# Kernel tuning notes

Measured on AMD Instinct MI355X. Metric: run time of the kernel, lower is better.

## Reference

```python
import jax, jax.numpy as jnp
import numpy as np

PI = np.pi
NDIMS, K, M, F = 3, 513, 65536, 16
H = (K - 1) // 2  # 256; augmented factor has K = 2*H + 1 rows


def setup_inputs() -> dict:
    key = jax.random.key(0)
    k1, k2, k3, k4 = jax.random.split(key, 4)
    x = jax.random.uniform(k1, (M, NDIMS), dtype=jnp.float32)          # samples in [0,1]
    factors_real = jax.random.uniform(k2, (NDIMS, H, F), dtype=jnp.float32)
    factors_imag = 0.1 * jax.random.uniform(k3, (NDIMS, H, F), dtype=jnp.float32)
    lam = jnp.full((F,), 1.0 / F, dtype=jnp.float32)                   # f_vec init in torch
    return {"x": x, "factors_real": factors_real, "factors_imag": factors_imag, "lam": lam}


def _augment(fr, fi):
    # aug_fac real = [R; ones; flip(R)], imag = [I; zeros; -flip(I)]  -> (NDIMS, K, F)
    ones = jnp.ones((NDIMS, 1, F), fr.dtype)
    zeros = jnp.zeros((NDIMS, 1, F), fi.dtype)
    Ar = jnp.concatenate([fr, ones, jnp.flip(fr, axis=1)], axis=1)
    Ai = jnp.concatenate([fi, zeros, -jnp.flip(fi, axis=1)], axis=1)
    return Ar, Ai


def _conditionals(Ar, Ai):
    # c[n, f] = 1 / trapz(relu(Re(bb1^T aug_fac_n))[:, f], t),  t = linspace(0.01, 1, 100)
    T = 100
    t = jnp.linspace(0.01, 1.0, T, dtype=jnp.float32)
    kv = jnp.arange(-H, H + 1, dtype=jnp.float32)
    phi = (2.0 * PI) * kv[:, None] * t[None, :]                         # (K, T)
    # bb1 = exp(-i*phi): Re(bb1^T (Ar + i Ai)) = cos(phi)^T Ar + sin(phi)^T Ai
    y = (jnp.einsum('kt,nkf->ntf', jnp.cos(phi), Ar)
         + jnp.einsum('kt,nkf->ntf', jnp.sin(phi), Ai))
    y = jnp.maximum(y, 0.0)
    dt = jnp.float32((1.0 - 0.01) / (T - 1))
    integral = 0.5 * jnp.sum(y[:, 1:, :] + y[:, :-1, :], axis=1) * dt   # (NDIMS, F)
    return 1.0 / integral


def reference(x, factors_real, factors_imag, lam):
    Ar, Ai = _augment(factors_real, factors_imag)
    # torch computes c from detached data (numpy trapz) -> constant w.r.t. grads
    c = jax.lax.stop_gradient(_conditionals(Ar, Ai))                    # (NDIMS, F)
    kv = jnp.arange(-H, H + 1, dtype=jnp.float32)
    # basis = exp(-i*2pi*k*x): Re(basis^T A) = cos^T Ar + sin^T Ai
    theta = (2.0 * PI) * kv[None, :, None] * jnp.swapaxes(x, 0, 1)[:, None, :]  # (NDIMS, K, M)
    proj = (jnp.einsum('nkm,nkf->nmf', jnp.cos(theta), Ar)
            + jnp.einsum('nkm,nkf->nmf', jnp.sin(theta), Ai))           # (NDIMS, M, F)
    proj = jnp.maximum(proj, 0.0) * c[:, None, :]
    res = jnp.prod(proj, axis=0)                                        # (M, F)
    # sum(res @ diagflat(lam), dim=1) == res @ lam
    return res @ lam
```

## Files before the change

### kernel.cpp

```cpp
#include <hip/hip_runtime.h>

#define NDIMS 3
#define H_HALF 256
#define F_DIM 16
#define PI_F 3.14159265358979323846f

typedef _Float16 half8_t __attribute__((ext_vector_type(8)));
typedef _Float16 h2 __attribute__((ext_vector_type(2)));
typedef __fp16 pk2_t __attribute__((ext_vector_type(2)));
typedef float float4_t __attribute__((ext_vector_type(4)));

#if __has_builtin(__builtin_amdgcn_fractf)
#define FRACT1(u) __builtin_amdgcn_fractf(u)
#else
#define FRACT1(u) ((u) - floorf(u))
#endif
#if __has_builtin(__builtin_amdgcn_sinf)
#define SIN2PI(u) __builtin_amdgcn_sinf(u)
#define COS2PI(u) __builtin_amdgcn_cosf(u)
#else
#define SIN2PI(u) __sinf(6.283185307f * (u))
#define COS2PI(u) __cosf(6.283185307f * (u))
#endif

static __device__ __forceinline__ unsigned int pk(float lo, float hi) {
    const pk2_t p = __builtin_amdgcn_cvt_pkrtz(lo, hi);
    return __builtin_bit_cast(unsigned int, p);
}
static __device__ __forceinline__ h2 pkh(float lo, float hi) {
    const pk2_t p = __builtin_amdgcn_cvt_pkrtz(lo, hi);
    return __builtin_bit_cast(h2, p);
}

__global__ __launch_bounds__(256) void cond_partial_kernel(const float* __restrict__ fr,
                                                           const float* __restrict__ fi,
                                                           float* __restrict__ part_out) {
    const int n = blockIdx.x / 7;
    const int chunk = blockIdx.x % 7;
    const int tid = threadIdx.x;
    const int f = tid & 15;
    const int tq = tid >> 4;
    const int t_idx = chunk * 16 + tq;
    const float t = 0.01f + 0.01f * (float)t_idx;
    const float beta = 2.f * PI_F * t;
    const float cb = __cosf(beta), sb = __sinf(beta);
    float cj = cb, sj = sb;
    const float* frn = fr + n * H_HALF * F_DIM + f;
    const float* fin = fi + n * H_HALF * F_DIM + f;
    float acc = 0.f;
    #pragma unroll 8
    for (int j = 1; j <= H_HALF; ++j) {
        const int h = H_HALF - j;
        acc = fmaf(cj, frn[h * F_DIM], acc);
        acc = fmaf(-sj, fin[h * F_DIM], acc);
        const float cn = fmaf(cj, cb, -sj * sb);
        const float sn = fmaf(sj, cb, cj * sb);
        cj = cn; sj = sn;
    }
    const float y = fmaxf(fmaf(2.f, acc, 1.f), 0.f);
    const float wgt = (t_idx == 0 || t_idx == 99) ? 0.005f : 0.01f;
    float contrib = (t_idx < 100) ? wgt * y : 0.f;
    contrib += __shfl_xor(contrib, 16, 64);
    contrib += __shfl_xor(contrib, 32, 64);
    __shared__ float red[4][16];
    const int wv = tid >> 6;
    const int lane = tid & 63;
    if (lane < 16) red[wv][lane] = contrib;
    __syncthreads();
    if (tid < 16) {
        part_out[blockIdx.x * 16 + tid] =
            (red[0][tid] + red[1][tid]) + (red[2][tid] + red[3][tid]);
    }
}

__global__ __launch_bounds__(512, 4) void main_kernel(const float* __restrict__ x,
                                                      const float* __restrict__ fr,
                                                      const float* __restrict__ fi,
                                                      const float* __restrict__ lam,
                                                      const float* __restrict__ part,
                                                      float* __restrict__ out) {
    __shared__ __align__(16) unsigned int Bls[48 * 260];
    const int tid = threadIdx.x;

    {
        const float4* fr4 = (const float4*)fr;
        const float4* fi4 = (const float4*)fi;
        #pragma unroll
        for (int r = 0; r < 6; ++r) {
            const int i4 = r * 512 + tid;
            const float4 a = fr4[i4];
            const float4 b = fi4[i4];
            const int n = i4 >> 10;
            const int h = (i4 >> 2) & 255;
            const int f0 = (i4 & 3) * 4;
            const int base = (n * 16 + f0) * 260 + (255 - h);
            Bls[base      ] = pk(a.x, -b.x);
            Bls[base + 260] = pk(a.y, -b.y);
            Bls[base + 520] = pk(a.z, -b.z);
            Bls[base + 780] = pk(a.w, -b.w);
        }
    }
    __syncthreads();

    const int wave = tid >> 6;
    const int lane = tid & 63;
    const int l15 = lane & 15;
    const int q = lane >> 4;
    const int mbase = (blockIdx.x * 8 + wave) * 16;

    const float xv0 = x[(mbase + l15) * 3 + 0];
    const float xv1 = x[(mbase + l15) * 3 + 1];
    const float xv2 = x[(mbase + l15) * 3 + 2];
    float psum[3];
    #pragma unroll
    for (int n = 0; n < 3; ++n) {
        float s = 0.f;
        #pragma unroll
        for (int c7 = 0; c7 < 7; ++c7) s += part[(n * 7 + c7) * 16 + l15];
        psum[n] = s;
    }
    const float lamv = lam[l15];

    float4_t accs[3];
    #pragma unroll
    for (int n = 0; n < 3; ++n) {
        const float xq = (n == 0) ? xv0 : (n == 1 ? xv1 : xv2);
        const float u1 = FRACT1(xq);
        const float cd1 = COS2PI(u1), sd1 = SIN2PI(u1);
        const float cd2 = fmaf(cd1, cd1, -sd1 * sd1), sd2 = 2.f * sd1 * cd1;
        const float cd3 = fmaf(cd2, cd1, -sd2 * sd1), sd3 = fmaf(sd2, cd1, cd2 * sd1);
        const h2 cc1 = pkh(cd1, cd1), ns1 = pkh(-sd1, sd1);
        const h2 cc2 = pkh(cd2, cd2), ns2 = pkh(-sd2, sd2);
        const h2 cc3 = pkh(cd3, cd3), ns3 = pkh(-sd3, sd3);
        const float ud = FRACT1(16.f * xq);
        const float cD = COS2PI(ud), sD = SIN2PI(ud);
        const float v0 = FRACT1((float)(q * 4 + 1) * xq);
        float c0 = COS2PI(v0), s0 = SIN2PI(v0);

        const unsigned int* Brow = &Bls[(n * 16 + l15) * 260 + q * 4];
        float4_t acc = {0.f, 0.f, 0.f, 0.f};
        #pragma unroll
        for (int s = 0; s < 16; ++s) {
            const int4 bv = *reinterpret_cast<const int4*>(Brow + s * 16);
            const half8_t bfrag = __builtin_bit_cast(half8_t, bv);
            const h2 b0 = pkh(c0, s0);
            const h2 bsw = pkh(s0, c0);
            const h2 d1 = __builtin_elementwise_fma(bsw, ns1, b0 * cc1);
            const h2 d2 = __builtin_elementwise_fma(bsw, ns2, b0 * cc2);
            const h2 d3 = __builtin_elementwise_fma(bsw, ns3, b0 * cc3);
            const int4 av = { __builtin_bit_cast(int, b0), __builtin_bit_cast(int, d1),
                              __builtin_bit_cast(int, d2), __builtin_bit_cast(int, d3) };
            const half8_t afrag = __builtin_bit_cast(half8_t, av);
            acc = __builtin_amdgcn_mfma_f32_16x16x32_f16(afrag, bfrag, acc, 0, 0, 0);
            const float t0 = fmaf(c0, cD, -s0 * sD);
            s0 = fmaf(s0, cD, c0 * sD);
            c0 = t0;
        }
        accs[n] = acc;
    }

    float r0 = 1.f, r1 = 1.f, r2 = 1.f, r3 = 1.f;
    #pragma unroll
    for (int n = 0; n < 3; ++n) {
        const float cc = 1.f / psum[n];
        r0 *= fmaxf(fmaf(2.f, accs[n][0], 1.f), 0.f) * cc;
        r1 *= fmaxf(fmaf(2.f, accs[n][1], 1.f), 0.f) * cc;
        r2 *= fmaxf(fmaf(2.f, accs[n][2], 1.f), 0.f) * cc;
        r3 *= fmaxf(fmaf(2.f, accs[n][3], 1.f), 0.f) * cc;
    }
    r0 *= lamv; r1 *= lamv; r2 *= lamv; r3 *= lamv;
    #pragma unroll
    for (int off = 1; off < 16; off <<= 1) {
        r0 += __shfl_xor(r0, off, 64);
        r1 += __shfl_xor(r1, off, 64);
        r2 += __shfl_xor(r2, off, 64);
        r3 += __shfl_xor(r3, off, 64);
    }
    if (l15 == 0) {
        float4 o = { r0, r1, r2, r3 };
        *reinterpret_cast<float4*>(out + mbase + q * 4) = o;
    }
}

extern "C" void kernel_launch(void* const* d_in, const int* in_sizes, int n_in,
                              void* d_out, int out_size, void* d_ws, size_t ws_size,
                              hipStream_t stream) {
    const float* x   = (const float*)d_in[0];
    const float* fr  = (const float*)d_in[1];
    const float* fi  = (const float*)d_in[2];
    const float* lam = (const float*)d_in[3];
    float* out = (float*)d_out;
    float* part = (float*)d_ws;

    const int M = in_sizes[0] / NDIMS;

    cond_partial_kernel<<<NDIMS * 7, 256, 0, stream>>>(fr, fi, part);
    main_kernel<<<M / 128, 512, 0, stream>>>(x, fr, fi, lam, part, out);
}
```

Before: 80.16 us.

## Fuse normalization-constant computation into main kernel via redundant MFMA tile pass

Drops the separate conditional-integral kernel. Each block of the main kernel now recomputes the 100-point trapezoid integrals itself, using the same MFMA tile routine with t values in place of x samples, and reduces them through shared memory. This removes one kernel launch and its serialization, but every block repeats the integral work (7 waves × 3 extra tile passes) and adds a barrier before the final product.

```diff
diff --git a/kernel.cpp b/kernel.cpp
--- a/kernel.cpp
+++ b/kernel.cpp
@@ -32,54 +32,49 @@
     return __builtin_bit_cast(h2, p);
 }
 
-__global__ __launch_bounds__(256) void cond_partial_kernel(const float* __restrict__ fr,
-                                                           const float* __restrict__ fi,
-                                                           float* __restrict__ part_out) {
-    const int n = blockIdx.x / 7;
-    const int chunk = blockIdx.x % 7;
-    const int tid = threadIdx.x;
-    const int f = tid & 15;
-    const int tq = tid >> 4;
-    const int t_idx = chunk * 16 + tq;
-    const float t = 0.01f + 0.01f * (float)t_idx;
-    const float beta = 2.f * PI_F * t;
-    const float cb = __cosf(beta), sb = __sinf(beta);
-    float cj = cb, sj = sb;
-    const float* frn = fr + n * H_HALF * F_DIM + f;
-    const float* fin = fi + n * H_HALF * F_DIM + f;
-    float acc = 0.f;
-    #pragma unroll 8
-    for (int j = 1; j <= H_HALF; ++j) {
-        const int h = H_HALF - j;
-        acc = fmaf(cj, frn[h * F_DIM], acc);
-        acc = fmaf(-sj, fin[h * F_DIM], acc);
-        const float cn = fmaf(cj, cb, -sj * sb);
-        const float sn = fmaf(sj, cb, cj * sb);
-        cj = cn; sj = sn;
+static __device__ __forceinline__ float4_t tile_pass(const float xq,
+                                                     const unsigned int* __restrict__ Brow,
+                                                     const int q) {
+    const float u1 = FRACT1(xq);
+    const float cd1 = COS2PI(u1), sd1 = SIN2PI(u1);
+    const float cd2 = fmaf(cd1, cd1, -sd1 * sd1), sd2 = 2.f * sd1 * cd1;
+    const float cd3 = fmaf(cd2, cd1, -sd2 * sd1), sd3 = fmaf(sd2, cd1, cd2 * sd1);
+    const h2 cc1 = pkh(cd1, cd1), ns1 = pkh(-sd1, sd1);
+    const h2 cc2 = pkh(cd2, cd2), ns2 = pkh(-sd2, sd2);
+    const h2 cc3 = pkh(cd3, cd3), ns3 = pkh(-sd3, sd3);
+    const float ud = FRACT1(16.f * xq);
+    const float cD = COS2PI(ud), sD = SIN2PI(ud);
+    const float v0 = FRACT1((float)(q * 4 + 1) * xq);
+    float c0 = COS2PI(v0), s0 = SIN2PI(v0);
+
+    float4_t acc = {0.f, 0.f, 0.f, 0.f};
+    #pragma unroll
+    for (int s = 0; s < 16; ++s) {
+        const int4 bv = *reinterpret_cast<const int4*>(Brow + s * 16);
+        const half8_t bfrag = __builtin_bit_cast(half8_t, bv);
+        const h2 b0 = pkh(c0, s0);
+        const h2 bsw = pkh(s0, c0);
+        const h2 d1 = __builtin_elementwise_fma(bsw, ns1, b0 * cc1);
+        const h2 d2 = __builtin_elementwise_fma(bsw, ns2, b0 * cc2);
+        const h2 d3 = __builtin_elementwise_fma(bsw, ns3, b0 * cc3);
+        const int4 av = { __builtin_bit_cast(int, b0), __builtin_bit_cast(int, d1),
+                          __builtin_bit_cast(int, d2), __builtin_bit_cast(int, d3) };
+        const half8_t afrag = __builtin_bit_cast(half8_t, av);
+        acc = __builtin_amdgcn_mfma_f32_16x16x32_f16(afrag, bfrag, acc, 0, 0, 0);
+        const float t0 = fmaf(c0, cD, -s0 * sD);
+        s0 = fmaf(s0, cD, c0 * sD);
+        c0 = t0;
     }
-    const float y = fmaxf(fmaf(2.f, acc, 1.f), 0.f);
-    const float wgt = (t_idx == 0 || t_idx == 99) ? 0.005f : 0.01f;
-    float contrib = (t_idx < 100) ? wgt * y : 0.f;
-    contrib += __shfl_xor(contrib, 16, 64);
-    contrib += __shfl_xor(contrib, 32, 64);
-    __shared__ float red[4][16];
-    const int wv = tid >> 6;
-    const int lane = tid & 63;
-    if (lane < 16) red[wv][lane] = contrib;
-    __syncthreads();
-    if (tid < 16) {
-        part_out[blockIdx.x * 16 + tid] =
-            (red[0][tid] + red[1][tid]) + (red[2][tid] + red[3][tid]);
-    }
+    return acc;
 }
 
 __global__ __launch_bounds__(512, 4) void main_kernel(const float* __restrict__ x,
                                                       const float* __restrict__ fr,
                                                       const float* __restrict__ fi,
                                                       const float* __restrict__ lam,
-                                                      const float* __restrict__ part,
                                                       float* __restrict__ out) {
     __shared__ __align__(16) unsigned int Bls[48 * 260];
+    __shared__ float red[NDIMS][7][16];
     const int tid = threadIdx.x;
 
     {
@@ -111,58 +106,52 @@
     const float xv0 = x[(mbase + l15) * 3 + 0];
     const float xv1 = x[(mbase + l15) * 3 + 1];
     const float xv2 = x[(mbase + l15) * 3 + 2];
-    float psum[3];
-    #pragma unroll
-    for (int n = 0; n < 3; ++n) {
-        float s = 0.f;
+    const float lamv = lam[l15];
+
+    if (wave < 7) {
+        const float tv = 0.01f + 0.01f * (float)(wave * 16 + l15);
         #pragma unroll
-        for (int c7 = 0; c7 < 7; ++c7) s += part[(n * 7 + c7) * 16 + l15];
-        psum[n] = s;
+        for (int n = 0; n < 3; ++n) {
+            const unsigned int* Brow = &Bls[(n * 16 + l15) * 260 + q * 4];
+            const float4_t ca = tile_pass(tv, Brow, q);
+            float contrib = 0.f;
+            #pragma unroll
+            for (int i = 0; i < 4; ++i) {
+                const int ti = wave * 16 + q * 4 + i;
+                const float y = fmaxf(fmaf(2.f, ca[i], 1.f), 0.f);
+                const float w = (ti == 0 || ti == 99) ? 0.005f
+                                                      : (ti < 100 ? 0.01f : 0.f);
+                contrib = fmaf(w, y, contrib);
+            }
+            contrib += __shfl_xor(contrib, 16, 64);
+            contrib += __shfl_xor(contrib, 32, 64);
+            if (lane < 16) red[n][wave][lane] = contrib;
+        }
     }
-    const float lamv = lam[l15];
 
     float4_t accs[3];
     #pragma unroll
     for (int n = 0; n < 3; ++n) {
         const float xq = (n == 0) ? xv0 : (n == 1 ? xv1 : xv2);
-        const float u1 = FRACT1(xq);
-        const float cd1 = COS2PI(u1), sd1 = SIN2PI(u1);
-        const float cd2 = fmaf(cd1, cd1, -sd1 * sd1), sd2 = 2.f * sd1 * cd1;
-        const float cd3 = fmaf(cd2, cd1, -sd2 * sd1), sd3 = fmaf(sd2, cd1, cd2 * sd1);
-        const h2 cc1 = pkh(cd1, cd1), ns1 = pkh(-sd1, sd1);
-        const h2 cc2 = pkh(cd2, cd2), ns2 = pkh(-sd2, sd2);
-        const h2 cc3 = pkh(cd3, cd3), ns3 = pkh(-sd3, sd3);
-        const float ud = FRACT1(16.f * xq);
-        const float cD = COS2PI(ud), sD = SIN2PI(ud);
-        const float v0 = FRACT1((float)(q * 4 + 1) * xq);
-        float c0 = COS2PI(v0), s0 = SIN2PI(v0);
+        const unsigned int* Brow = &Bls[(n * 16 + l15) * 260 + q * 4];
+        accs[n] = tile_pass(xq, Brow, q);
+    }
 
-        const unsigned int* Brow = &Bls[(n * 16 + l15) * 260 + q * 4];
-        float4_t acc = {0.f, 0.f, 0.f, 0.f};
+    __syncthreads();
+
+    float cinv[3];
+    #pragma unroll
+    for (int n = 0; n < 3; ++n) {
+        float s = 0.f;
         #pragma unroll
-        for (int s = 0; s < 16; ++s) {
-            const int4 bv = *reinterpret_cast<const int4*>(Brow + s * 16);
-            const half8_t bfrag = __builtin_bit_cast(half8_t, bv);
-            const h2 b0 = pkh(c0, s0);
-            const h2 bsw = pkh(s0, c0);
-            const h2 d1 = __builtin_elementwise_fma(bsw, ns1, b0 * cc1);
-            const h2 d2 = __builtin_elementwise_fma(bsw, ns2, b0 * cc2);
-            const h2 d3 = __builtin_elementwise_fma(bsw, ns3, b0 * cc3);
-            const int4 av = { __builtin_bit_cast(int, b0), __builtin_bit_cast(int, d1),
-                              __builtin_bit_cast(int, d2), __builtin_bit_cast(int, d3) };
-            const half8_t afrag = __builtin_bit_cast(half8_t, av);
-            acc = __builtin_amdgcn_mfma_f32_16x16x32_f16(afrag, bfrag, acc, 0, 0, 0);
-            const float t0 = fmaf(c0, cD, -s0 * sD);
-            s0 = fmaf(s0, cD, c0 * sD);
-            c0 = t0;
-        }
-        accs[n] = acc;
+        for (int w = 0; w < 7; ++w) s += red[n][w][l15];
+        cinv[n] = 1.f / s;
     }
 
     float r0 = 1.f, r1 = 1.f, r2 = 1.f, r3 = 1.f;
     #pragma unroll
     for (int n = 0; n < 3; ++n) {
-        const float cc = 1.f / psum[n];
+        const float cc = cinv[n];
         r0 *= fmaxf(fmaf(2.f, accs[n][0], 1.f), 0.f) * cc;
         r1 *= fmaxf(fmaf(2.f, accs[n][1], 1.f), 0.f) * cc;
         r2 *= fmaxf(fmaf(2.f, accs[n][2], 1.f), 0.f) * cc;
@@ -190,10 +179,9 @@
     const float* fi  = (const float*)d_in[2];
     const float* lam = (const float*)d_in[3];
     float* out = (float*)d_out;
-    float* part = (float*)d_ws;
+    (void)d_ws; (void)ws_size;
 
     const int M = in_sizes[0] / NDIMS;
 
-    cond_partial_kernel<<<NDIMS * 7, 256, 0, stream>>>(fr, fi, part);
-    main_kernel<<<M / 128, 512, 0, stream>>>(x, fr, fi, lam, part, out);
+    main_kernel<<<M / 128, 512, 0, stream>>>(x, fr, fi, lam, out);
 }
```

Measured after the change: 71.10 us. -11.3%, faster.
